# Kernel optimization log

Measured on AMD Instinct MI355X. Metric: run time of the kernel, lower is better.

The kernel has to match this reference:

```python
import jax, jax.numpy as jnp
import numpy as np

N_NODES = 100000
N_EDGES = 1600000
IN_CH = 128
HID = 32
N_GRAPHS = 64


def _gcn_conv(x, src, dst, W, b, n_nodes):
    # PyG GCNConv defaults: x' = D^{-1/2} (A + I) D^{-1/2} (x W) + b
    h = x @ W                                   # [N, out]
    loop = jnp.arange(n_nodes, dtype=src.dtype)
    s = jnp.concatenate([src, loop])            # add self-loops
    d = jnp.concatenate([dst, loop])
    deg = jax.ops.segment_sum(jnp.ones_like(d, dtype=h.dtype), d, num_segments=n_nodes)
    dinv = jnp.where(deg > 0, jax.lax.rsqrt(deg), 0.0)
    norm = dinv[s] * dinv[d]                    # [E+N]
    msg = h[s] * norm[:, None]                  # gather + scale
    out = jax.ops.segment_sum(msg, d, num_segments=n_nodes)  # scatter-add
    return out + b


def setup_inputs() -> dict:
    key = jax.random.key(0)
    ks = jax.random.split(key, 8)
    x = jax.random.normal(ks[0], (N_NODES, IN_CH), dtype=jnp.float32)
    edge_index = jax.random.randint(ks[1], (2, N_EDGES), 0, N_NODES, dtype=jnp.int32)
    batch = jnp.sort(jax.random.randint(ks[2], (N_NODES,), 0, N_GRAPHS, dtype=jnp.int32))
    W1 = jax.random.normal(ks[3], (IN_CH, HID), dtype=jnp.float32) * (1.0 / np.sqrt(IN_CH))
    b1 = jnp.zeros((HID,), dtype=jnp.float32)
    W2 = jax.random.normal(ks[4], (HID, HID), dtype=jnp.float32) * (1.0 / np.sqrt(HID))
    b2 = jnp.zeros((HID,), dtype=jnp.float32)
    Ws = jax.random.normal(ks[5], (HID, HID), dtype=jnp.float32) * (1.0 / np.sqrt(HID))
    bs = jnp.zeros((HID,), dtype=jnp.float32)
    return {"x": x, "edge_index": edge_index, "batch": batch,
            "W1": W1, "b1": b1, "W2": W2, "b2": b2, "Ws": Ws, "bs": bs}


def reference(x, edge_index, batch, W1, b1, W2, b2, Ws, bs):
    src, dst = edge_index[0], edge_index[1]
    n = x.shape[0]
    h = _gcn_conv(x, src, dst, W1, b1, n)
    h = jax.nn.relu(h)
    h = _gcn_conv(h, src, dst, W2, b2, n)       # [N, HID] node embeddings
    # global_mean_pool over graph ids
    ones = jnp.ones((n,), dtype=h.dtype)
    cnt = jax.ops.segment_sum(ones, batch, num_segments=N_GRAPHS)
    gsum = jax.ops.segment_sum(h, batch, num_segments=N_GRAPHS)
    g = gsum / jnp.maximum(cnt, 1.0)[:, None]   # [G, HID]
    summary = g @ Ws + bs
    return summary, h
```

## Files before the change

kernel.cpp:

```cpp
#include <hip/hip_runtime.h>

#define N_NODES  100000
#define N_EDGES  1600000
#define IN_CH    128
#define HID      32
#define N_GRAPHS 64

#define NBIN   391
#define CHUNK  4096
#define MGRID  391
#define STG    5120
#define LCAP   2048

#define OFF_B      0
#define OFF_EDGEPK 3200000
#define OFF_CSR    4800000
#define OFF_COLT   6400000
#define OFF_BINB   6400391
#define OFF_ROWPTR 6400784
#define OFF_DINV   6500785

__device__ __forceinline__ unsigned bfr(float f) {
    unsigned u = __float_as_uint(f);
    u += 0x7fffu + ((u >> 16) & 1u);
    return u >> 16;
}
__device__ __forceinline__ float bflo(unsigned w) { return __uint_as_float(w << 16); }
__device__ __forceinline__ float bfhi(unsigned w) { return __uint_as_float(w & 0xffff0000u); }

__global__ __launch_bounds__(512) void hist_kernel(const int* __restrict__ dst,
                                                   int* __restrict__ H) {
    __shared__ int s[512];
    int t = threadIdx.x, wg = blockIdx.x;
    s[t] = 0;
    __syncthreads();
    int e0 = wg * CHUNK, e1 = min(e0 + CHUNK, N_EDGES);
    for (int e = e0 + t; e < e1; e += 512) {
        int d = dst[e];
        if ((unsigned)d < N_NODES) atomicAdd(&s[d >> 8], 1);
    }
    __syncthreads();
    if (t < NBIN) H[t * MGRID + wg] = s[t];
}

__global__ __launch_bounds__(512) void scanrow_kernel(int* __restrict__ H,
                                                      int* __restrict__ colT) {
    __shared__ int s[512];
    int t = threadIdx.x, bin = blockIdx.x;
    s[t] = (t < MGRID) ? H[bin * MGRID + t] : 0;
    __syncthreads();
    for (int off = 1; off < 512; off <<= 1) {
        int v = (t >= off) ? s[t - off] : 0;
        __syncthreads();
        if (t >= off) s[t] += v;
        __syncthreads();
    }
    if (t < MGRID) H[bin * MGRID + t] = t ? s[t - 1] : 0;
    if (t == 0) colT[bin] = s[MGRID - 1];
}

__global__ __launch_bounds__(512) void scanbase_kernel(const int* __restrict__ colT,
                                                       int* __restrict__ binB,
                                                       int* __restrict__ row_ptr) {
    __shared__ int s[512];
    int t = threadIdx.x;
    s[t] = (t < NBIN) ? colT[t] : 0;
    __syncthreads();
    for (int off = 1; off < 512; off <<= 1) {
        int v = (t >= off) ? s[t - off] : 0;
        __syncthreads();
        if (t >= off) s[t] += v;
        __syncthreads();
    }
    if (t < NBIN) binB[t] = t ? s[t - 1] : 0;
    if (t == 0) { binB[NBIN] = s[NBIN - 1]; row_ptr[N_NODES] = s[NBIN - 1]; }
}

__global__ __launch_bounds__(512) void msplit_kernel(const int* __restrict__ src,
                                                     const int* __restrict__ dst,
                                                     const int* __restrict__ H,
                                                     const int* __restrict__ binB,
                                                     int* __restrict__ edgepk) {
    __shared__ int s[512];
    __shared__ int cur[NBIN];
    __shared__ int gb[NBIN];
    __shared__ int stage[CHUNK];
    __shared__ int gof[CHUNK];
    int t = threadIdx.x, wg = blockIdx.x;
    s[t] = 0;
    __syncthreads();
    int e0 = wg * CHUNK, e1 = min(e0 + CHUNK, N_EDGES);
    for (int e = e0 + t; e < e1; e += 512) {
        int d = dst[e];
        if ((unsigned)d < N_NODES) atomicAdd(&s[d >> 8], 1);
    }
    __syncthreads();
    for (int off = 1; off < 512; off <<= 1) {
        int v = (t >= off) ? s[t - off] : 0;
        __syncthreads();
        if (t >= off) s[t] += v;
        __syncthreads();
    }
    if (t < NBIN) {
        int lo = t ? s[t - 1] : 0;
        cur[t] = lo;
        gb[t] = binB[t] + H[t * MGRID + wg] - lo;
    }
    __syncthreads();
    for (int e = e0 + t; e < e1; e += 512) {
        int d = dst[e];
        if ((unsigned)d < N_NODES) {
            int b = d >> 8;
            int p = atomicAdd(&cur[b], 1);
            stage[p] = (src[e] << 8) | (d & 255);
            gof[p] = gb[b];
        }
    }
    __syncthreads();
    int total = s[511];
    for (int p = t; p < total; p += 512)
        edgepk[gof[p] + p] = stage[p];
}

__global__ __launch_bounds__(256) void csr2_kernel(const int* __restrict__ edgepk,
                                                   const int* __restrict__ binB,
                                                   int* __restrict__ row_ptr,
                                                   float* __restrict__ dinv,
                                                   int* __restrict__ csr) {
    __shared__ int cnt[256], s[256], cur[256];
    __shared__ int stage[STG];
    int t = threadIdx.x, bin = blockIdx.x;
    int ebase = binB[bin], eend = binB[bin + 1];
    int n = eend - ebase;
    cnt[t] = 0;
    __syncthreads();
    for (int p = ebase + t; p < eend; p += 256)
        atomicAdd(&cnt[edgepk[p] & 255], 1);
    __syncthreads();
    s[t] = cnt[t];
    __syncthreads();
    for (int off = 1; off < 256; off <<= 1) {
        int v = (t >= off) ? s[t - off] : 0;
        __syncthreads();
        if (t >= off) s[t] += v;
        __syncthreads();
    }
    int excl = t ? s[t - 1] : 0;
    int node = (bin << 8) + t;
    if (node < N_NODES) {
        dinv[node] = rsqrtf((float)(cnt[t] + 1));
        row_ptr[node] = ebase + excl;
    }
    cur[t] = excl;
    __syncthreads();
    for (int p = ebase + t; p < eend; p += 256) {
        int w = edgepk[p];
        int l = atomicAdd(&cur[w & 255], 1);
        int sv = w >> 8;
        if (l < STG) stage[l] = sv;
        else csr[ebase + l] = sv;
    }
    __syncthreads();
    int lim = min(n, STG);
    for (int l = t; l < lim; l += 256)
        csr[ebase + l] = stage[l];
}

#define XS1 132
__global__ __launch_bounds__(256) void gemm1_kernel(const float* __restrict__ x,
                                                    const float* __restrict__ W1,
                                                    const float* __restrict__ dinv,
                                                    unsigned* __restrict__ Bu) {
    __shared__ float Wl[IN_CH * HID];
    __shared__ float xs[32 * XS1];
    int tid = threadIdx.x;
    for (int j = tid; j < IN_CH * HID / 4; j += 256)
        ((float4*)Wl)[j] = ((const float4*)W1)[j];
    int row0 = blockIdx.x * 32;
    const float4* x4 = (const float4*)(x + (size_t)row0 * IN_CH);
    for (int j = tid; j < 32 * IN_CH / 4; j += 256) {
        int r = j >> 5, k4 = j & 31;
        ((float4*)&xs[r * XS1])[k4] = x4[j];
    }
    __syncthreads();
    int r = tid >> 3, cg = (tid & 7) * 4;
    const float* xr = &xs[r * XS1];
    float4 acc = {0.f, 0.f, 0.f, 0.f};
    #pragma unroll 8
    for (int k = 0; k < IN_CH; ++k) {
        float xv = xr[k];
        float4 w = *(const float4*)&Wl[k * HID + cg];
        acc.x += xv * w.x; acc.y += xv * w.y; acc.z += xv * w.z; acc.w += xv * w.w;
    }
    int row = row0 + r;
    float dv = dinv[row];
    uint2 p;
    p.x = bfr(acc.x * dv) | (bfr(acc.y * dv) << 16);
    p.y = bfr(acc.z * dv) | (bfr(acc.w * dv) << 16);
    *(uint2*)&Bu[(size_t)row * 16 + (tid & 7) * 2] = p;
}

#define XS2 36
__global__ __launch_bounds__(256) void gemm2_kernel(const float* __restrict__ in,
                                                    const float* __restrict__ W2,
                                                    const float* __restrict__ dinv,
                                                    unsigned* __restrict__ Bu) {
    __shared__ float Wl[HID * HID];
    __shared__ float xs[32 * XS2];
    int tid = threadIdx.x;
    ((float4*)Wl)[tid] = ((const float4*)W2)[tid];
    int row0 = blockIdx.x * 32;
    const float4* in4 = (const float4*)(in + (size_t)row0 * HID);
    {
        int r = tid >> 3, k4 = tid & 7;
        ((float4*)&xs[r * XS2])[k4] = in4[tid];
    }
    __syncthreads();
    int r = tid >> 3, cg = (tid & 7) * 4;
    const float* xr = &xs[r * XS2];
    float4 acc = {0.f, 0.f, 0.f, 0.f};
    #pragma unroll
    for (int k = 0; k < HID; ++k) {
        float xv = xr[k];
        float4 w = *(const float4*)&Wl[k * HID + cg];
        acc.x += xv * w.x; acc.y += xv * w.y; acc.z += xv * w.z; acc.w += xv * w.w;
    }
    int row = row0 + r;
    float dv = dinv[row];
    uint2 p;
    p.x = bfr(acc.x * dv) | (bfr(acc.y * dv) << 16);
    p.y = bfr(acc.z * dv) | (bfr(acc.w * dv) << 16);
    *(uint2*)&Bu[(size_t)row * 16 + (tid & 7) * 2] = p;
}

__global__ __launch_bounds__(256) void layer_kernel(const unsigned* __restrict__ Bu,
                                                    const int* __restrict__ csr,
                                                    const int* __restrict__ row_ptr,
                                                    const float* __restrict__ dinv,
                                                    const float* __restrict__ bias,
                                                    float* __restrict__ out,
                                                    int relu) {
    __shared__ int sidx[LCAP];
    int tid = threadIdx.x;
    int n0 = blockIdx.x * 64;
    int nend = min(n0 + 64, N_NODES);
    int j0 = row_ptr[n0], j1 = row_ptr[nend];
    int nblk = j1 - j0;
    int staged = (nblk <= LCAP);
    if (staged)
        for (int p = tid; p < nblk; p += 256) sidx[p] = csr[j0 + p];
    __syncthreads();
    int node = n0 + (tid >> 2);
    if (node >= N_NODES) return;
    int c4 = tid & 3;
    const uint4* Br = (const uint4*)Bu;
    uint4 sw = Br[(size_t)node * 4 + c4];
    float a0 = bflo(sw.x), a1 = bfhi(sw.x);
    float a2 = bflo(sw.y), a3 = bfhi(sw.y);
    float a4 = bflo(sw.z), a5 = bfhi(sw.z);
    float a6 = bflo(sw.w), a7 = bfhi(sw.w);
    if (staged) {
        int j = row_ptr[node] - j0, re = row_ptr[node + 1] - j0;
        for (; j + 8 <= re; j += 8) {
            int s0 = sidx[j + 0], s1 = sidx[j + 1], s2 = sidx[j + 2], s3 = sidx[j + 3];
            int s4 = sidx[j + 4], s5 = sidx[j + 5], s6 = sidx[j + 6], s7 = sidx[j + 7];
            uint4 w0 = Br[(size_t)s0 * 4 + c4], w1 = Br[(size_t)s1 * 4 + c4];
            uint4 w2 = Br[(size_t)s2 * 4 + c4], w3 = Br[(size_t)s3 * 4 + c4];
            uint4 w4 = Br[(size_t)s4 * 4 + c4], w5 = Br[(size_t)s5 * 4 + c4];
            uint4 w6 = Br[(size_t)s6 * 4 + c4], w7 = Br[(size_t)s7 * 4 + c4];
            a0 += ((bflo(w0.x) + bflo(w1.x)) + (bflo(w2.x) + bflo(w3.x)))
                + ((bflo(w4.x) + bflo(w5.x)) + (bflo(w6.x) + bflo(w7.x)));
            a1 += ((bfhi(w0.x) + bfhi(w1.x)) + (bfhi(w2.x) + bfhi(w3.x)))
                + ((bfhi(w4.x) + bfhi(w5.x)) + (bfhi(w6.x) + bfhi(w7.x)));
            a2 += ((bflo(w0.y) + bflo(w1.y)) + (bflo(w2.y) + bflo(w3.y)))
                + ((bflo(w4.y) + bflo(w5.y)) + (bflo(w6.y) + bflo(w7.y)));
            a3 += ((bfhi(w0.y) + bfhi(w1.y)) + (bfhi(w2.y) + bfhi(w3.y)))
                + ((bfhi(w4.y) + bfhi(w5.y)) + (bfhi(w6.y) + bfhi(w7.y)));
            a4 += ((bflo(w0.z) + bflo(w1.z)) + (bflo(w2.z) + bflo(w3.z)))
                + ((bflo(w4.z) + bflo(w5.z)) + (bflo(w6.z) + bflo(w7.z)));
            a5 += ((bfhi(w0.z) + bfhi(w1.z)) + (bfhi(w2.z) + bfhi(w3.z)))
                + ((bfhi(w4.z) + bfhi(w5.z)) + (bfhi(w6.z) + bfhi(w7.z)));
            a6 += ((bflo(w0.w) + bflo(w1.w)) + (bflo(w2.w) + bflo(w3.w)))
                + ((bflo(w4.w) + bflo(w5.w)) + (bflo(w6.w) + bflo(w7.w)));
            a7 += ((bfhi(w0.w) + bfhi(w1.w)) + (bfhi(w2.w) + bfhi(w3.w)))
                + ((bfhi(w4.w) + bfhi(w5.w)) + (bfhi(w6.w) + bfhi(w7.w)));
        }
        if (j + 4 <= re) {
            int s0 = sidx[j], s1 = sidx[j + 1], s2 = sidx[j + 2], s3 = sidx[j + 3];
            uint4 w0 = Br[(size_t)s0 * 4 + c4], w1 = Br[(size_t)s1 * 4 + c4];
            uint4 w2 = Br[(size_t)s2 * 4 + c4], w3 = Br[(size_t)s3 * 4 + c4];
            a0 += (bflo(w0.x) + bflo(w1.x)) + (bflo(w2.x) + bflo(w3.x));
            a1 += (bfhi(w0.x) + bfhi(w1.x)) + (bfhi(w2.x) + bfhi(w3.x));
            a2 += (bflo(w0.y) + bflo(w1.y)) + (bflo(w2.y) + bflo(w3.y));
            a3 += (bfhi(w0.y) + bfhi(w1.y)) + (bfhi(w2.y) + bfhi(w3.y));
            a4 += (bflo(w0.z) + bflo(w1.z)) + (bflo(w2.z) + bflo(w3.z));
            a5 += (bfhi(w0.z) + bfhi(w1.z)) + (bfhi(w2.z) + bfhi(w3.z));
            a6 += (bflo(w0.w) + bflo(w1.w)) + (bflo(w2.w) + bflo(w3.w));
            a7 += (bfhi(w0.w) + bfhi(w1.w)) + (bfhi(w2.w) + bfhi(w3.w));
            j += 4;
        }
        for (; j < re; ++j) {
            uint4 w = Br[(size_t)sidx[j] * 4 + c4];
            a0 += bflo(w.x); a1 += bfhi(w.x);
            a2 += bflo(w.y); a3 += bfhi(w.y);
            a4 += bflo(w.z); a5 += bfhi(w.z);
            a6 += bflo(w.w); a7 += bfhi(w.w);
        }
    } else {
        int j = row_ptr[node], re = row_ptr[node + 1];
        for (; j < re; ++j) {
            uint4 w = Br[(size_t)csr[j] * 4 + c4];
            a0 += bflo(w.x); a1 += bfhi(w.x);
            a2 += bflo(w.y); a3 += bfhi(w.y);
            a4 += bflo(w.z); a5 += bfhi(w.z);
            a6 += bflo(w.w); a7 += bfhi(w.w);
        }
    }
    float dv = dinv[node];
    float4 bA = *(const float4*)&bias[8 * c4];
    float4 bB = *(const float4*)&bias[8 * c4 + 4];
    float4 o1, o2;
    o1.x = a0 * dv + bA.x; o1.y = a1 * dv + bA.y;
    o1.z = a2 * dv + bA.z; o1.w = a3 * dv + bA.w;
    o2.x = a4 * dv + bB.x; o2.y = a5 * dv + bB.y;
    o2.z = a6 * dv + bB.z; o2.w = a7 * dv + bB.w;
    if (relu) {
        o1.x = fmaxf(o1.x, 0.f); o1.y = fmaxf(o1.y, 0.f);
        o1.z = fmaxf(o1.z, 0.f); o1.w = fmaxf(o1.w, 0.f);
        o2.x = fmaxf(o2.x, 0.f); o2.y = fmaxf(o2.y, 0.f);
        o2.z = fmaxf(o2.z, 0.f); o2.w = fmaxf(o2.w, 0.f);
    }
    float* orow = out + (size_t)node * HID + 8 * c4;
    *(float4*)orow = o1;
    *(float4*)(orow + 4) = o2;
}

__global__ __launch_bounds__(256) void pool_kernel(const float* __restrict__ h,
                                                   const int* __restrict__ batch,
                                                   float* __restrict__ gsum,
                                                   float* __restrict__ cnt) {
    __shared__ float pool[N_GRAPHS * HID];
    __shared__ float cntl[N_GRAPHS];
    __shared__ int gmin, gmax;
    int t = threadIdx.x;
    for (int j = t; j < N_GRAPHS * HID; j += 256) pool[j] = 0.f;
    if (t < N_GRAPHS) cntl[t] = 0.f;
    if (t == 0) { gmin = N_GRAPHS; gmax = -1; }
    __syncthreads();
    int start = blockIdx.x * 256;
    int end = min(start + 256, N_NODES);
    int c = t & 31;
    float racc = 0.f;
    int rg = -1, rcnt = 0;
    for (int nb = start + (t >> 5); nb < end; nb += 8) {
        float v = h[(size_t)nb * HID + c];
        int g = batch[nb];
        if (g != rg) {
            if ((unsigned)rg < N_GRAPHS) {
                atomicAdd(&pool[rg * HID + c], racc);
                if (c == 0) {
                    atomicAdd(&cntl[rg], (float)rcnt);
                    atomicMin(&gmin, rg); atomicMax(&gmax, rg);
                }
            }
            rg = g; racc = v; rcnt = 1;
        } else { racc += v; ++rcnt; }
    }
    if ((unsigned)rg < N_GRAPHS) {
        atomicAdd(&pool[rg * HID + c], racc);
        if (c == 0) {
            atomicAdd(&cntl[rg], (float)rcnt);
            atomicMin(&gmin, rg); atomicMax(&gmax, rg);
        }
    }
    __syncthreads();
    int lo = gmin, hi = gmax;
    if (hi >= lo) {
        int span = (hi - lo + 1) * HID;
        for (int j = t; j < span; j += 256)
            atomicAdd(&gsum[lo * HID + j], pool[lo * HID + j]);
        for (int j = t; j <= hi - lo; j += 256)
            atomicAdd(&cnt[lo + j], cntl[lo + j]);
    }
}

__global__ void summary_kernel(const float* __restrict__ gsum, const float* __restrict__ cnt,
                               const float* __restrict__ Ws, const float* __restrict__ bs,
                               float* __restrict__ out) {
    int g = blockIdx.x, c = threadIdx.x;
    float inv = 1.f / fmaxf(cnt[g], 1.f);
    float acc = bs[c];
    #pragma unroll
    for (int k = 0; k < HID; ++k)
        acc += gsum[g * HID + k] * inv * Ws[k * HID + c];
    out[g * HID + c] = acc;
}

extern "C" void kernel_launch(void* const* d_in, const int* in_sizes, int n_in,
                              void* d_out, int out_size, void* d_ws, size_t ws_size,
                              hipStream_t stream) {
    const float* x    = (const float*)d_in[0];
    const int* edge   = (const int*)d_in[1];
    const int* src    = edge;
    const int* dst    = edge + N_EDGES;
    const int* batch  = (const int*)d_in[2];
    const float* W1   = (const float*)d_in[3];
    const float* b1   = (const float*)d_in[4];
    const float* W2   = (const float*)d_in[5];
    const float* b2   = (const float*)d_in[6];
    const float* Ws   = (const float*)d_in[7];
    const float* bs   = (const float*)d_in[8];

    float* ws      = (float*)d_ws;
    unsigned* Bu   = (unsigned*)(ws + OFF_B);
    int*   H       = (int*)(ws + OFF_B);
    int*   edgepk  = (int*)(ws + OFF_EDGEPK);
    int*   csr     = (int*)(ws + OFF_CSR);
    int*   colT    = (int*)(ws + OFF_COLT);
    int*   binB    = (int*)(ws + OFF_BINB);
    int*   row_ptr = (int*)(ws + OFF_ROWPTR);
    float* dinv    = ws + OFF_DINV;
    float* gsum    = ws + OFF_EDGEPK;
    float* cnt     = gsum + N_GRAPHS * HID;

    float* out     = (float*)d_out;
    float* out_sum = out;
    float* out_h   = out + N_GRAPHS * HID;

    hist_kernel    <<<MGRID, 512, 0, stream>>>(dst, H);
    scanrow_kernel <<<NBIN,  512, 0, stream>>>(H, colT);
    scanbase_kernel<<<1,     512, 0, stream>>>(colT, binB, row_ptr);
    msplit_kernel  <<<MGRID, 512, 0, stream>>>(src, dst, H, binB, edgepk);
    csr2_kernel    <<<NBIN,  256, 0, stream>>>(edgepk, binB, row_ptr, dinv, csr);

    int lgrid = (N_NODES + 63) / 64;

    gemm1_kernel<<<N_NODES / 32, 256, 0, stream>>>(x, W1, dinv, Bu);
    layer_kernel<<<lgrid, 256, 0, stream>>>(Bu, csr, row_ptr, dinv, b1, out_h, 1);

    gemm2_kernel<<<N_NODES / 32, 256, 0, stream>>>(out_h, W2, dinv, Bu);
    layer_kernel<<<lgrid, 256, 0, stream>>>(Bu, csr, row_ptr, dinv, b2, out_h, 0);

    hipMemsetAsync(gsum, 0, (N_GRAPHS * HID + N_GRAPHS) * sizeof(float), stream);
    pool_kernel<<<NBIN, 256, 0, stream>>>(out_h, batch, gsum, cnt);
    summary_kernel<<<N_GRAPHS, HID, 0, stream>>>(gsum, cnt, Ws, bs, out_sum);
}
```

Measured before the change: 227.0 us.

## Fuse CSR build kernels into one cooperative kernel with grid syncs

Replaces the five separate kernels that build the CSR (histogram, row scan, base scan, multi-split, per-bin CSR) with one cooperative kernel that separates phases with grid.sync. The per-block bin histogram is kept in shared memory rather than recomputed, so dst is read one time fewer. The gsum/cnt memset is also folded into gemm1's first block, which removes a memset call. This trades several launch boundaries for grid-wide barriers, and it requires all 391 blocks of 512 threads to be co-resident.

```diff
diff --git a/kernel.cpp b/kernel.cpp
--- a/kernel.cpp
+++ b/kernel.cpp
@@ -1,4 +1,7 @@
 #include <hip/hip_runtime.h>
+#include <hip/hip_cooperative_groups.h>
+
+namespace cg = cooperative_groups;
 
 #define N_NODES  100000
 #define N_EDGES  1600000
@@ -28,10 +31,23 @@
 __device__ __forceinline__ float bflo(unsigned w) { return __uint_as_float(w << 16); }
 __device__ __forceinline__ float bfhi(unsigned w) { return __uint_as_float(w & 0xffff0000u); }
 
-__global__ __launch_bounds__(512) void hist_kernel(const int* __restrict__ dst,
-                                                   int* __restrict__ H) {
+__global__ __launch_bounds__(512) void build_kernel(const int* __restrict__ src,
+                                                    const int* __restrict__ dst,
+                                                    int* __restrict__ H,
+                                                    int* __restrict__ colT,
+                                                    int* __restrict__ binB,
+                                                    int* __restrict__ row_ptr,
+                                                    float* __restrict__ dinv,
+                                                    int* __restrict__ edgepk,
+                                                    int* __restrict__ csr) {
     __shared__ int s[512];
+    __shared__ int s2[512];
+    __shared__ int curA[NBIN];
+    __shared__ int gb[NBIN];
+    __shared__ int shpool[2 * CHUNK];
+    cg::grid_group grid = cg::this_grid();
     int t = threadIdx.x, wg = blockIdx.x;
+
     s[t] = 0;
     __syncthreads();
     int e0 = wg * CHUNK, e1 = min(e0 + CHUNK, N_EDGES);
@@ -41,77 +57,53 @@
     }
     __syncthreads();
     if (t < NBIN) H[t * MGRID + wg] = s[t];
-}
-
-__global__ __launch_bounds__(512) void scanrow_kernel(int* __restrict__ H,
-                                                      int* __restrict__ colT) {
-    __shared__ int s[512];
-    int t = threadIdx.x, bin = blockIdx.x;
-    s[t] = (t < MGRID) ? H[bin * MGRID + t] : 0;
-    __syncthreads();
+    grid.sync();
+
+    s2[t] = (t < MGRID) ? H[wg * MGRID + t] : 0;
+    __syncthreads();
+    for (int off = 1; off < 512; off <<= 1) {
+        int v = (t >= off) ? s2[t - off] : 0;
+        __syncthreads();
+        if (t >= off) s2[t] += v;
+        __syncthreads();
+    }
+    if (t < MGRID) H[wg * MGRID + t] = t ? s2[t - 1] : 0;
+    if (t == 0) colT[wg] = s2[MGRID - 1];
+    grid.sync();
+
+    if (wg == 0) {
+        s2[t] = (t < NBIN) ? colT[t] : 0;
+        __syncthreads();
+        for (int off = 1; off < 512; off <<= 1) {
+            int v = (t >= off) ? s2[t - off] : 0;
+            __syncthreads();
+            if (t >= off) s2[t] += v;
+            __syncthreads();
+        }
+        if (t < NBIN) binB[t] = t ? s2[t - 1] : 0;
+        if (t == 0) { binB[NBIN] = s2[NBIN - 1]; row_ptr[N_NODES] = s2[NBIN - 1]; }
+    }
+    grid.sync();
+
     for (int off = 1; off < 512; off <<= 1) {
         int v = (t >= off) ? s[t - off] : 0;
         __syncthreads();
         if (t >= off) s[t] += v;
         __syncthreads();
     }
-    if (t < MGRID) H[bin * MGRID + t] = t ? s[t - 1] : 0;
-    if (t == 0) colT[bin] = s[MGRID - 1];
-}
-
-__global__ __launch_bounds__(512) void scanbase_kernel(const int* __restrict__ colT,
-                                                       int* __restrict__ binB,
-                                                       int* __restrict__ row_ptr) {
-    __shared__ int s[512];
-    int t = threadIdx.x;
-    s[t] = (t < NBIN) ? colT[t] : 0;
-    __syncthreads();
-    for (int off = 1; off < 512; off <<= 1) {
-        int v = (t >= off) ? s[t - off] : 0;
-        __syncthreads();
-        if (t >= off) s[t] += v;
-        __syncthreads();
-    }
-    if (t < NBIN) binB[t] = t ? s[t - 1] : 0;
-    if (t == 0) { binB[NBIN] = s[NBIN - 1]; row_ptr[N_NODES] = s[NBIN - 1]; }
-}
-
-__global__ __launch_bounds__(512) void msplit_kernel(const int* __restrict__ src,
-                                                     const int* __restrict__ dst,
-                                                     const int* __restrict__ H,
-                                                     const int* __restrict__ binB,
-                                                     int* __restrict__ edgepk) {
-    __shared__ int s[512];
-    __shared__ int cur[NBIN];
-    __shared__ int gb[NBIN];
-    __shared__ int stage[CHUNK];
-    __shared__ int gof[CHUNK];
-    int t = threadIdx.x, wg = blockIdx.x;
-    s[t] = 0;
-    __syncthreads();
-    int e0 = wg * CHUNK, e1 = min(e0 + CHUNK, N_EDGES);
-    for (int e = e0 + t; e < e1; e += 512) {
-        int d = dst[e];
-        if ((unsigned)d < N_NODES) atomicAdd(&s[d >> 8], 1);
-    }
-    __syncthreads();
-    for (int off = 1; off < 512; off <<= 1) {
-        int v = (t >= off) ? s[t - off] : 0;
-        __syncthreads();
-        if (t >= off) s[t] += v;
-        __syncthreads();
-    }
     if (t < NBIN) {
         int lo = t ? s[t - 1] : 0;
-        cur[t] = lo;
+        curA[t] = lo;
         gb[t] = binB[t] + H[t * MGRID + wg] - lo;
     }
     __syncthreads();
+    int* stage = shpool;
+    int* gof   = shpool + CHUNK;
     for (int e = e0 + t; e < e1; e += 512) {
         int d = dst[e];
         if ((unsigned)d < N_NODES) {
             int b = d >> 8;
-            int p = atomicAdd(&cur[b], 1);
+            int p = atomicAdd(&curA[b], 1);
             stage[p] = (src[e] << 8) | (d & 255);
             gof[p] = gb[b];
         }
@@ -120,60 +112,57 @@
     int total = s[511];
     for (int p = t; p < total; p += 512)
         edgepk[gof[p] + p] = stage[p];
-}
-
-__global__ __launch_bounds__(256) void csr2_kernel(const int* __restrict__ edgepk,
-                                                   const int* __restrict__ binB,
-                                                   int* __restrict__ row_ptr,
-                                                   float* __restrict__ dinv,
-                                                   int* __restrict__ csr) {
-    __shared__ int cnt[256], s[256], cur[256];
-    __shared__ int stage[STG];
-    int t = threadIdx.x, bin = blockIdx.x;
-    int ebase = binB[bin], eend = binB[bin + 1];
+    grid.sync();
+
+    int ebase = binB[wg], eend = binB[wg + 1];
     int n = eend - ebase;
-    cnt[t] = 0;
-    __syncthreads();
-    for (int p = ebase + t; p < eend; p += 256)
-        atomicAdd(&cnt[edgepk[p] & 255], 1);
-    __syncthreads();
-    s[t] = cnt[t];
+    if (t < 256) curA[t] = 0;
+    __syncthreads();
+    for (int p = ebase + t; p < eend; p += 512)
+        atomicAdd(&curA[edgepk[p] & 255], 1);
+    __syncthreads();
+    if (t < 256) s2[t] = curA[t];
     __syncthreads();
     for (int off = 1; off < 256; off <<= 1) {
-        int v = (t >= off) ? s[t - off] : 0;
-        __syncthreads();
-        if (t >= off) s[t] += v;
-        __syncthreads();
-    }
-    int excl = t ? s[t - 1] : 0;
-    int node = (bin << 8) + t;
-    if (node < N_NODES) {
-        dinv[node] = rsqrtf((float)(cnt[t] + 1));
-        row_ptr[node] = ebase + excl;
-    }
-    cur[t] = excl;
-    __syncthreads();
-    for (int p = ebase + t; p < eend; p += 256) {
+        int v = (t >= off && t < 256) ? s2[t - off] : 0;
+        __syncthreads();
+        if (t >= off && t < 256) s2[t] += v;
+        __syncthreads();
+    }
+    if (t < 256) {
+        int excl = t ? s2[t - 1] : 0;
+        int node = (wg << 8) + t;
+        if (node < N_NODES) {
+            dinv[node] = rsqrtf((float)(curA[t] + 1));
+            row_ptr[node] = ebase + excl;
+        }
+        gb[t] = excl;
+    }
+    __syncthreads();
+    for (int p = ebase + t; p < eend; p += 512) {
         int w = edgepk[p];
-        int l = atomicAdd(&cur[w & 255], 1);
+        int l = atomicAdd(&gb[w & 255], 1);
         int sv = w >> 8;
-        if (l < STG) stage[l] = sv;
+        if (l < STG) shpool[l] = sv;
         else csr[ebase + l] = sv;
     }
     __syncthreads();
     int lim = min(n, STG);
-    for (int l = t; l < lim; l += 256)
-        csr[ebase + l] = stage[l];
+    for (int l = t; l < lim; l += 512)
+        csr[ebase + l] = shpool[l];
 }
 
 #define XS1 132
 __global__ __launch_bounds__(256) void gemm1_kernel(const float* __restrict__ x,
                                                     const float* __restrict__ W1,
                                                     const float* __restrict__ dinv,
-                                                    unsigned* __restrict__ Bu) {
+                                                    unsigned* __restrict__ Bu,
+                                                    float* __restrict__ gz) {
     __shared__ float Wl[IN_CH * HID];
     __shared__ float xs[32 * XS1];
     int tid = threadIdx.x;
+    if (blockIdx.x == 0)
+        for (int q = tid; q < N_GRAPHS * HID + N_GRAPHS; q += 256) gz[q] = 0.f;
     for (int j = tid; j < IN_CH * HID / 4; j += 256)
         ((float4*)Wl)[j] = ((const float4*)W1)[j];
     int row0 = blockIdx.x * 32;
@@ -183,13 +172,13 @@
         ((float4*)&xs[r * XS1])[k4] = x4[j];
     }
     __syncthreads();
-    int r = tid >> 3, cg = (tid & 7) * 4;
+    int r = tid >> 3, cg_ = (tid & 7) * 4;
     const float* xr = &xs[r * XS1];
     float4 acc = {0.f, 0.f, 0.f, 0.f};
     #pragma unroll 8
     for (int k = 0; k < IN_CH; ++k) {
         float xv = xr[k];
-        float4 w = *(const float4*)&Wl[k * HID + cg];
+        float4 w = *(const float4*)&Wl[k * HID + cg_];
         acc.x += xv * w.x; acc.y += xv * w.y; acc.z += xv * w.z; acc.w += xv * w.w;
     }
     int row = row0 + r;
@@ -216,13 +205,13 @@
         ((float4*)&xs[r * XS2])[k4] = in4[tid];
     }
     __syncthreads();
-    int r = tid >> 3, cg = (tid & 7) * 4;
+    int r = tid >> 3, cg_ = (tid & 7) * 4;
     const float* xr = &xs[r * XS2];
     float4 acc = {0.f, 0.f, 0.f, 0.f};
     #pragma unroll
     for (int k = 0; k < HID; ++k) {
         float xv = xr[k];
-        float4 w = *(const float4*)&Wl[k * HID + cg];
+        float4 w = *(const float4*)&Wl[k * HID + cg_];
         acc.x += xv * w.x; acc.y += xv * w.y; acc.z += xv * w.z; acc.w += xv * w.w;
     }
     int row = row0 + r;
@@ -427,21 +416,20 @@
     float* out_sum = out;
     float* out_h   = out + N_GRAPHS * HID;
 
-    hist_kernel    <<<MGRID, 512, 0, stream>>>(dst, H);
-    scanrow_kernel <<<NBIN,  512, 0, stream>>>(H, colT);
-    scanbase_kernel<<<1,     512, 0, stream>>>(colT, binB, row_ptr);
-    msplit_kernel  <<<MGRID, 512, 0, stream>>>(src, dst, H, binB, edgepk);
-    csr2_kernel    <<<NBIN,  256, 0, stream>>>(edgepk, binB, row_ptr, dinv, csr);
+    void* bargs[] = { (void*)&src, (void*)&dst, (void*)&H, (void*)&colT,
+                      (void*)&binB, (void*)&row_ptr, (void*)&dinv,
+                      (void*)&edgepk, (void*)&csr };
+    hipLaunchCooperativeKernel((const void*)build_kernel, dim3(MGRID), dim3(512),
+                               bargs, 0, stream);
 
     int lgrid = (N_NODES + 63) / 64;
 
-    gemm1_kernel<<<N_NODES / 32, 256, 0, stream>>>(x, W1, dinv, Bu);
+    gemm1_kernel<<<N_NODES / 32, 256, 0, stream>>>(x, W1, dinv, Bu, gsum);
     layer_kernel<<<lgrid, 256, 0, stream>>>(Bu, csr, row_ptr, dinv, b1, out_h, 1);
 
     gemm2_kernel<<<N_NODES / 32, 256, 0, stream>>>(out_h, W2, dinv, Bu);
     layer_kernel<<<lgrid, 256, 0, stream>>>(Bu, csr, row_ptr, dinv, b2, out_h, 0);
 
-    hipMemsetAsync(gsum, 0, (N_GRAPHS * HID + N_GRAPHS) * sizeof(float), stream);
     pool_kernel<<<NBIN, 256, 0, stream>>>(out_h, batch, gsum, cnt);
     summary_kernel<<<N_GRAPHS, HID, 0, stream>>>(gsum, cnt, Ws, bs, out_sum);
 }
```

Result: slower. 431.6 us (+90.2%).
